# Kernel tuning notes

Hardware: AMD Instinct MI355X
Metric: run time of the kernel (lower is better)

The kernel has to match this reference:

```python
import jax, jax.numpy as jnp
import numpy as np

N_NODES = 100000
N_EDGES = 1600000
D_IN = 64
D_OUT = 64


def setup_inputs() -> dict:
    key = jax.random.key(0)
    k1, k2, k3, k4, k5 = jax.random.split(key, 5)
    x = jax.random.normal(k1, (N_NODES, D_IN), dtype=jnp.float32)
    edge_index = jax.random.randint(k2, (2, N_EDGES), 0, N_NODES, dtype=jnp.int64)
    dist_vec = jax.random.uniform(k3, (N_EDGES,), dtype=jnp.float32)
    # Linear params (xavier-uniform-like scale for W)
    limit = float(np.sqrt(6.0 / (D_IN + D_OUT)))
    W = jax.random.uniform(k4, (D_OUT, D_IN), minval=-limit, maxval=limit, dtype=jnp.float32)
    b = jax.random.uniform(k5, (D_OUT,), minval=-limit, maxval=limit, dtype=jnp.float32)
    return {"x": x, "edge_index": edge_index, "dist_vec": dist_vec, "W": W, "b": b}


def reference(x, edge_index, dist_vec, W, b):
    row, col = edge_index[0], edge_index[1]
    n = x.shape[0]
    # degree of destination (col) nodes
    deg = jax.ops.segment_sum(jnp.ones_like(dist_vec), col, num_segments=n)
    deg_inv_sqrt = jnp.where(deg > 0, jax.lax.rsqrt(deg), 0.0)
    norm = deg_inv_sqrt[row] * deg_inv_sqrt[col]  # [E]
    w = jnp.exp(-dist_vec ** 2) * norm            # [E]
    # sparse.mm(adj, x): out[row] += w * x[col]
    msgs = w[:, None] * x[col]                    # [E, D_IN]
    side_embed = jax.ops.segment_sum(msgs, row, num_segments=n)  # [N, D_IN]
    return side_embed @ W.T + b
```

## Files before the change

### kernel.cpp

```cpp
#include <hip/hip_runtime.h>
#include <hip/hip_fp16.h>


constexpr int NN   = 100000;
constexpr int NE   = 1600000;
constexpr int D    = 64;
constexpr int NRB  = (NN + 63) / 64;
constexpr int NCB  = (NN + 255) / 256;
constexpr int HB   = 250;
constexpr int HT   = 1024;
constexpr int CHUNK = NE / HB;
constexpr int NSR  = NRB * HB;
constexpr int NSCC = NCB * HB;
constexpr int NST  = NSR + NSCC;
constexpr int SCB  = 1024;
constexpr int SCG  = (NST + SCB - 1) / SCB;
constexpr int CAP  = 1536;

using f16x8 = __attribute__((ext_vector_type(8))) _Float16;
using f32x4 = __attribute__((ext_vector_type(4))) float;

__global__ void __launch_bounds__(HT)
hist2_kernel(const int* __restrict__ row, const int* __restrict__ col,
             int* __restrict__ hist) {
    __shared__ int hr[NRB], hc[NCB];
    const int t = threadIdx.x;
    for (int i = t; i < NRB; i += HT) hr[i] = 0;
    for (int i = t; i < NCB; i += HT) hc[i] = 0;
    __syncthreads();
    const int e0 = blockIdx.x * CHUNK;
    for (int e = e0 + t * 4; e < e0 + CHUNK; e += HT * 4) {
        const int4 r4 = *reinterpret_cast<const int4*>(row + e);
        const int4 c4 = *reinterpret_cast<const int4*>(col + e);
        atomicAdd(&hr[r4.x >> 6], 1); atomicAdd(&hr[r4.y >> 6], 1);
        atomicAdd(&hr[r4.z >> 6], 1); atomicAdd(&hr[r4.w >> 6], 1);
        atomicAdd(&hc[c4.x >> 8], 1); atomicAdd(&hc[c4.y >> 8], 1);
        atomicAdd(&hc[c4.z >> 8], 1); atomicAdd(&hc[c4.w >> 8], 1);
    }
    __syncthreads();
    for (int i = t; i < NRB; i += HT) hist[i * HB + blockIdx.x] = hr[i];
    for (int i = t; i < NCB; i += HT) hist[NSR + i * HB + blockIdx.x] = hc[i];
}

__global__ void scanpart_kernel(const int* __restrict__ a, int* __restrict__ bsum) {
    __shared__ int red[16];
    const int t = threadIdx.x;
    const int i = blockIdx.x * SCB + t;
    int s = (i < NST) ? a[i] : 0;
    #pragma unroll
    for (int o = 1; o < 64; o <<= 1) s += __shfl_xor(s, o);
    if ((t & 63) == 0) red[t >> 6] = s;
    __syncthreads();
    if (t < 16) {
        int ss = red[t];
        #pragma unroll
        for (int o = 1; o < 16; o <<= 1) ss += __shfl_xor(ss, o);
        if (t == 0) bsum[blockIdx.x] = ss;
    }
}

__global__ void scanfinal_kernel(int* __restrict__ a, const int* __restrict__ bsum) {
    __shared__ int wsum[16], wsum2[16], red[16];
    __shared__ int prefix_s;
    const int t = threadIdx.x;
    const int i = blockIdx.x * SCB + t;
    const int lane = t & 63;
    const int w = t >> 6;
    int pv = (t < blockIdx.x) ? bsum[t] : 0;
    #pragma unroll
    for (int o = 1; o < 64; o <<= 1) pv += __shfl_xor(pv, o);
    if (lane == 0) red[w] = pv;
    const int v = (i < NST) ? a[i] : 0;
    int s = v;
    #pragma unroll
    for (int o = 1; o < 64; o <<= 1) { int u = __shfl_up(s, o); if (lane >= o) s += u; }
    if (lane == 63) wsum[w] = s;
    __syncthreads();
    if (t < 16) {
        int ss = wsum[t];
        #pragma unroll
        for (int o = 1; o < 16; o <<= 1) { int u = __shfl_up(ss, o); if (t >= o) ss += u; }
        wsum2[t] = ss;
        int rr = red[t];
        #pragma unroll
        for (int o = 1; o < 16; o <<= 1) rr += __shfl_xor(rr, o);
        if (t == 0) prefix_s = rr;
    }
    __syncthreads();
    const int excl = prefix_s + (w ? wsum2[w - 1] : 0) + (s - v);
    if (i < NST) a[i] = excl;
}

__global__ void __launch_bounds__(HT)
scatboth_kernel(const int* __restrict__ row, const int* __restrict__ col,
                const float* __restrict__ dist, const int* __restrict__ hoff,
                unsigned* __restrict__ payload, unsigned char* __restrict__ colidx) {
    __shared__ int cur_r[NRB];
    __shared__ int cur_c[NCB];
    const int t = threadIdx.x;
    for (int i = t; i < NRB; i += HT) cur_r[i] = hoff[i * HB + blockIdx.x];
    for (int i = t; i < NCB; i += HT) cur_c[i] = hoff[NSR + i * HB + blockIdx.x] - NE;
    __syncthreads();
    const int e0 = blockIdx.x * CHUNK;
    for (int e = e0 + t * 4; e < e0 + CHUNK; e += HT * 4) {
        const int4 r4 = *reinterpret_cast<const int4*>(row + e);
        const int4 c4 = *reinterpret_cast<const int4*>(col + e);
        const float4 d4 = *reinterpret_cast<const float4*>(dist + e);
        const int rr[4] = {r4.x, r4.y, r4.z, r4.w};
        const int cc[4] = {c4.x, c4.y, c4.z, c4.w};
        const float dd[4] = {d4.x, d4.y, d4.z, d4.w};
        #pragma unroll
        for (int j = 0; j < 4; ++j) {
            const int r = rr[j];
            const int c = cc[j];
            const float dv = dd[j];
            const unsigned w8 = (unsigned)(__expf(-dv * dv) * 255.0f + 0.5f);
            const int pr = atomicAdd(&cur_r[r >> 6], 1);
            payload[pr] = ((unsigned)(r & 63) << 25) | (w8 << 17) | (unsigned)c;
            const int pc = atomicAdd(&cur_c[c >> 8], 1);
            colidx[pc] = (unsigned char)(c & 255);
        }
    }
}

__global__ void __launch_bounds__(256)
coldinv_kernel(const int* __restrict__ hoff, const unsigned char* __restrict__ colidx,
               float* __restrict__ dinv) {
    __shared__ int cnt[256];
    const int t = threadIdx.x;
    const int b = blockIdx.x;
    cnt[t] = 0;
    __syncthreads();
    const int s0 = hoff[NSR + b * HB] - NE;
    const int s1 = (b + 1 < NCB) ? (hoff[NSR + (b + 1) * HB] - NE) : NE;
    for (int k = s0 + t; k < s1; k += 256) atomicAdd(&cnt[colidx[k]], 1);
    __syncthreads();
    const int n = b * 256 + t;
    if (n < NN) {
        const int d = cnt[t];
        dinv[n] = (d > 0) ? rsqrtf((float)d) : 0.0f;
    }
}

__global__ void __launch_bounds__(256)
ygemm_kernel(const float* __restrict__ x, const float* __restrict__ W,
             __half* __restrict__ y) {
    const int t = threadIdx.x;
    const int m  = t & 15;
    const int kb = (t & 63) >> 4;
    f16x8 bf[4][2];
    #pragma unroll
    for (int jt = 0; jt < 4; ++jt) {
        #pragma unroll
        for (int kh = 0; kh < 2; ++kh) {
            const float* wp = W + (size_t)(jt * 16 + m) * 64 + kh * 32 + kb * 8;
            const float4 w0 = *reinterpret_cast<const float4*>(wp);
            const float4 w1 = *reinterpret_cast<const float4*>(wp + 4);
            f16x8 f;
            f[0] = (_Float16)w0.x; f[1] = (_Float16)w0.y;
            f[2] = (_Float16)w0.z; f[3] = (_Float16)w0.w;
            f[4] = (_Float16)w1.x; f[5] = (_Float16)w1.y;
            f[6] = (_Float16)w1.z; f[7] = (_Float16)w1.w;
            bf[jt][kh] = f;
        }
    }
    const int wid = (blockIdx.x * 256 + t) >> 6;
    const int nw  = (gridDim.x * 256) >> 6;
    for (int nt = wid; nt < NN / 16; nt += nw) {
        const int n0 = nt * 16;
        f16x8 af[2];
        #pragma unroll
        for (int kh = 0; kh < 2; ++kh) {
            const float* xp = x + (size_t)(n0 + m) * 64 + kh * 32 + kb * 8;
            const float4 x0 = *reinterpret_cast<const float4*>(xp);
            const float4 x1 = *reinterpret_cast<const float4*>(xp + 4);
            f16x8 f;
            f[0] = (_Float16)x0.x; f[1] = (_Float16)x0.y;
            f[2] = (_Float16)x0.z; f[3] = (_Float16)x0.w;
            f[4] = (_Float16)x1.x; f[5] = (_Float16)x1.y;
            f[6] = (_Float16)x1.z; f[7] = (_Float16)x1.w;
            af[kh] = f;
        }
        #pragma unroll
        for (int jt = 0; jt < 4; ++jt) {
            f32x4 acc = {0.f, 0.f, 0.f, 0.f};
            acc = __builtin_amdgcn_mfma_f32_16x16x32_f16(bf[jt][0], af[0], acc, 0, 0, 0);
            acc = __builtin_amdgcn_mfma_f32_16x16x32_f16(bf[jt][1], af[1], acc, 0, 0, 0);
            const size_t elem = (size_t)(n0 + m) * 64 + jt * 16 + kb * 4;
            union { uint2 u; __half h[4]; } pk;
            pk.h[0] = __float2half(acc[0]); pk.h[1] = __float2half(acc[1]);
            pk.h[2] = __float2half(acc[2]); pk.h[3] = __float2half(acc[3]);
            *reinterpret_cast<uint2*>(y + elem) = pk.u;
        }
    }
}

__global__ void __launch_bounds__(256)
gather_fused_kernel(const int* __restrict__ hoff, const unsigned* __restrict__ payload,
                    const float* __restrict__ dinvg, const __half* __restrict__ y,
                    const float* __restrict__ bias, float* __restrict__ out) {
    __shared__ unsigned stage[CAP];
    __shared__ unsigned sorted[CAP];
    __shared__ int cnt[64], cur[64], rs[65];
    __shared__ float dinv_s[64];
    const int t = threadIdx.x;
    const int lane = t & 63;
    const int wv = t >> 6;
    const int b = blockIdx.x;
    const int sub = lane >> 3;
    const int ch8 = (lane & 7) << 3;
    constexpr float WSCL = 1.0f / 255.0f;
    const float4 b0 = *reinterpret_cast<const float4*>(bias + ch8);
    const float4 b1 = *reinterpret_cast<const float4*>(bias + ch8 + 4);

    if (t < 64) {
        cnt[t] = 0;
        const int n = b * 64 + t;
        dinv_s[t] = (n < NN) ? dinvg[n] : 0.0f;
    }
    const int s0g = hoff[b * HB];
    const int s1g = (b + 1 < NRB) ? hoff[(b + 1) * HB] : NE;
    int ne = s1g - s0g;
    ne = (ne < CAP) ? ne : CAP;
    __syncthreads();
    for (int k = t; k < ne; k += 256) {
        const unsigned p = payload[s0g + k];
        stage[k] = p;
        atomicAdd(&cnt[p >> 25], 1);
    }
    __syncthreads();
    if (t < 64) {
        const int v = cnt[t];
        int s = v;
        #pragma unroll
        for (int o = 1; o < 64; o <<= 1) { int u = __shfl_up(s, o); if (t >= o) s += u; }
        cur[t] = s - v;
        rs[t] = s - v;
        if (t == 63) rs[64] = s;
    }
    __syncthreads();
    for (int k = t; k < ne; k += 256) {
        const unsigned p = stage[k];
        const int pos = atomicAdd(&cur[p >> 25], 1);
        sorted[pos] = p;
    }
    __syncthreads();

    for (int ln = wv; ln < 64; ln += 4) {
        const int n = b * 64 + ln;
        if (n >= NN) break;
        const int e0 = rs[ln];
        const int e1 = rs[ln + 1];
        float a0 = 0.f, a1 = 0.f, a2 = 0.f, a3 = 0.f;
        float a4 = 0.f, a5 = 0.f, a6 = 0.f, a7 = 0.f;
        for (int p0 = e0; p0 < e1; p0 += 8) {
            const int pp = p0 + sub;
            const int ppc = (pp < e1) ? pp : (e1 - 1);
            const unsigned m = sorted[ppc];
            const int c = (int)(m & 0x1FFFFu);
            float wgt = (float)((m >> 17) & 255u) * WSCL * dinvg[c];
            wgt = (pp < e1) ? wgt : 0.0f;
            const float4 raw = *reinterpret_cast<const float4*>(y + (size_t)c * 64 + ch8);
            const __half2* h2 = reinterpret_cast<const __half2*>(&raw);
            const float2 f0 = __half22float2(h2[0]);
            const float2 f1 = __half22float2(h2[1]);
            const float2 f2 = __half22float2(h2[2]);
            const float2 f3 = __half22float2(h2[3]);
            a0 += wgt * f0.x; a1 += wgt * f0.y; a2 += wgt * f1.x; a3 += wgt * f1.y;
            a4 += wgt * f2.x; a5 += wgt * f2.y; a6 += wgt * f3.x; a7 += wgt * f3.y;
        }
        #pragma unroll
        for (int o = 8; o < 64; o <<= 1) {
            a0 += __shfl_xor(a0, o); a1 += __shfl_xor(a1, o);
            a2 += __shfl_xor(a2, o); a3 += __shfl_xor(a3, o);
            a4 += __shfl_xor(a4, o); a5 += __shfl_xor(a5, o);
            a6 += __shfl_xor(a6, o); a7 += __shfl_xor(a7, o);
        }
        if (sub == 0) {
            const float dn = dinv_s[ln];
            const float4 o0 = make_float4(b0.x + dn * a0, b0.y + dn * a1,
                                          b0.z + dn * a2, b0.w + dn * a3);
            const float4 o1 = make_float4(b1.x + dn * a4, b1.y + dn * a5,
                                          b1.z + dn * a6, b1.w + dn * a7);
            float* op = out + (size_t)n * 64 + ch8;
            *reinterpret_cast<float4*>(op)     = o0;
            *reinterpret_cast<float4*>(op + 4) = o1;
        }
    }
}

extern "C" void kernel_launch(void* const* d_in, const int* in_sizes, int n_in,
                              void* d_out, int out_size, void* d_ws, size_t ws_size,
                              hipStream_t stream) {
    const float* x    = (const float*)d_in[0];
    const int*   ei   = (const int*)d_in[1];
    const float* dist = (const float*)d_in[2];
    const float* W    = (const float*)d_in[3];
    const float* b    = (const float*)d_in[4];
    float* out = (float*)d_out;

    const int* row = ei;
    const int* col = ei + NE;

    unsigned*      payload = (unsigned*)d_ws;
    __half*        y       = (__half*)(payload + NE);
    int*           hist    = (int*)(y + (size_t)NN * 64);
    int*           bsum    = hist + NST;
    unsigned char* colidx  = (unsigned char*)(bsum + SCG);
    float*         dinv    = (float*)(colidx + NE);

    ygemm_kernel    <<<1024, 256, 0, stream>>>(x, W, y);
    hist2_kernel    <<<HB, HT, 0, stream>>>(row, col, hist);
    scanpart_kernel <<<SCG, SCB, 0, stream>>>(hist, bsum);
    scanfinal_kernel<<<SCG, SCB, 0, stream>>>(hist, bsum);
    scatboth_kernel <<<HB, HT, 0, stream>>>(row, col, dist, hist, payload, colidx);
    coldinv_kernel  <<<NCB, 256, 0, stream>>>(hist, colidx, dinv);
    gather_fused_kernel<<<NRB, 256, 0, stream>>>(hist, payload, dinv, y, b, out);
}
```

Before: 117.5 us.

## Merge y-GEMM and edge histogram into one horizontally fused prep kernel

Combines the independent x·W^T fp16 MFMA kernel and the row/col block histogram kernel into a single launch. The first 250 blocks build the histograms and the next 512 blocks run the GEMM, so both independent jobs share the device at the same time and one launch is removed. Block size drops from 1024/256 to 512 for both roles. The histogram blocks now have fewer threads per chunk, and register pressure from the MFMA path may now apply to the histogram blocks as well.

```diff
diff --git a/kernel.cpp b/kernel.cpp
--- a/kernel.cpp
+++ b/kernel.cpp
@@ -9,6 +9,8 @@
 constexpr int NCB  = (NN + 255) / 256;
 constexpr int HB   = 250;
 constexpr int HT   = 1024;
+constexpr int PT   = 512;
+constexpr int YGB  = 512;
 constexpr int CHUNK = NE / HB;
 constexpr int NSR  = NRB * HB;
 constexpr int NSCC = NCB * HB;
@@ -20,26 +22,78 @@
 using f16x8 = __attribute__((ext_vector_type(8))) _Float16;
 using f32x4 = __attribute__((ext_vector_type(4))) float;
 
-__global__ void __launch_bounds__(HT)
-hist2_kernel(const int* __restrict__ row, const int* __restrict__ col,
-             int* __restrict__ hist) {
+__global__ void __launch_bounds__(PT)
+prep_kernel(const float* __restrict__ x, const float* __restrict__ W,
+            __half* __restrict__ y, const int* __restrict__ row,
+            const int* __restrict__ col, int* __restrict__ hist) {
     __shared__ int hr[NRB], hc[NCB];
     const int t = threadIdx.x;
-    for (int i = t; i < NRB; i += HT) hr[i] = 0;
-    for (int i = t; i < NCB; i += HT) hc[i] = 0;
-    __syncthreads();
-    const int e0 = blockIdx.x * CHUNK;
-    for (int e = e0 + t * 4; e < e0 + CHUNK; e += HT * 4) {
-        const int4 r4 = *reinterpret_cast<const int4*>(row + e);
-        const int4 c4 = *reinterpret_cast<const int4*>(col + e);
-        atomicAdd(&hr[r4.x >> 6], 1); atomicAdd(&hr[r4.y >> 6], 1);
-        atomicAdd(&hr[r4.z >> 6], 1); atomicAdd(&hr[r4.w >> 6], 1);
-        atomicAdd(&hc[c4.x >> 8], 1); atomicAdd(&hc[c4.y >> 8], 1);
-        atomicAdd(&hc[c4.z >> 8], 1); atomicAdd(&hc[c4.w >> 8], 1);
-    }
-    __syncthreads();
-    for (int i = t; i < NRB; i += HT) hist[i * HB + blockIdx.x] = hr[i];
-    for (int i = t; i < NCB; i += HT) hist[NSR + i * HB + blockIdx.x] = hc[i];
+    const int blk = blockIdx.x;
+    if (blk < HB) {
+        for (int i = t; i < NRB; i += PT) hr[i] = 0;
+        for (int i = t; i < NCB; i += PT) hc[i] = 0;
+        __syncthreads();
+        const int e0 = blk * CHUNK;
+        for (int e = e0 + t * 4; e < e0 + CHUNK; e += PT * 4) {
+            const int4 r4 = *reinterpret_cast<const int4*>(row + e);
+            const int4 c4 = *reinterpret_cast<const int4*>(col + e);
+            atomicAdd(&hr[r4.x >> 6], 1); atomicAdd(&hr[r4.y >> 6], 1);
+            atomicAdd(&hr[r4.z >> 6], 1); atomicAdd(&hr[r4.w >> 6], 1);
+            atomicAdd(&hc[c4.x >> 8], 1); atomicAdd(&hc[c4.y >> 8], 1);
+            atomicAdd(&hc[c4.z >> 8], 1); atomicAdd(&hc[c4.w >> 8], 1);
+        }
+        __syncthreads();
+        for (int i = t; i < NRB; i += PT) hist[i * HB + blk] = hr[i];
+        for (int i = t; i < NCB; i += PT) hist[NSR + i * HB + blk] = hc[i];
+    } else {
+        const int m  = t & 15;
+        const int kb = (t & 63) >> 4;
+        f16x8 bf[4][2];
+        #pragma unroll
+        for (int jt = 0; jt < 4; ++jt) {
+            #pragma unroll
+            for (int kh = 0; kh < 2; ++kh) {
+                const float* wp = W + (size_t)(jt * 16 + m) * 64 + kh * 32 + kb * 8;
+                const float4 w0 = *reinterpret_cast<const float4*>(wp);
+                const float4 w1 = *reinterpret_cast<const float4*>(wp + 4);
+                f16x8 f;
+                f[0] = (_Float16)w0.x; f[1] = (_Float16)w0.y;
+                f[2] = (_Float16)w0.z; f[3] = (_Float16)w0.w;
+                f[4] = (_Float16)w1.x; f[5] = (_Float16)w1.y;
+                f[6] = (_Float16)w1.z; f[7] = (_Float16)w1.w;
+                bf[jt][kh] = f;
+            }
+        }
+        const int wid = ((blk - HB) * PT + t) >> 6;
+        const int nw  = (YGB * PT) >> 6;
+        for (int nt = wid; nt < NN / 16; nt += nw) {
+            const int n0 = nt * 16;
+            f16x8 af[2];
+            #pragma unroll
+            for (int kh = 0; kh < 2; ++kh) {
+                const float* xp = x + (size_t)(n0 + m) * 64 + kh * 32 + kb * 8;
+                const float4 x0 = *reinterpret_cast<const float4*>(xp);
+                const float4 x1 = *reinterpret_cast<const float4*>(xp + 4);
+                f16x8 f;
+                f[0] = (_Float16)x0.x; f[1] = (_Float16)x0.y;
+                f[2] = (_Float16)x0.z; f[3] = (_Float16)x0.w;
+                f[4] = (_Float16)x1.x; f[5] = (_Float16)x1.y;
+                f[6] = (_Float16)x1.z; f[7] = (_Float16)x1.w;
+                af[kh] = f;
+            }
+            #pragma unroll
+            for (int jt = 0; jt < 4; ++jt) {
+                f32x4 acc = {0.f, 0.f, 0.f, 0.f};
+                acc = __builtin_amdgcn_mfma_f32_16x16x32_f16(bf[jt][0], af[0], acc, 0, 0, 0);
+                acc = __builtin_amdgcn_mfma_f32_16x16x32_f16(bf[jt][1], af[1], acc, 0, 0, 0);
+                const size_t elem = (size_t)(n0 + m) * 64 + jt * 16 + kb * 4;
+                union { uint2 u; __half h[4]; } pk;
+                pk.h[0] = __float2half(acc[0]); pk.h[1] = __float2half(acc[1]);
+                pk.h[2] = __float2half(acc[2]); pk.h[3] = __float2half(acc[3]);
+                *reinterpret_cast<uint2*>(y + elem) = pk.u;
+            }
+        }
+    }
 }
 
 __global__ void scanpart_kernel(const int* __restrict__ a, int* __restrict__ bsum) {
@@ -139,59 +193,6 @@
     if (n < NN) {
         const int d = cnt[t];
         dinv[n] = (d > 0) ? rsqrtf((float)d) : 0.0f;
-    }
-}
-
-__global__ void __launch_bounds__(256)
-ygemm_kernel(const float* __restrict__ x, const float* __restrict__ W,
-             __half* __restrict__ y) {
-    const int t = threadIdx.x;
-    const int m  = t & 15;
-    const int kb = (t & 63) >> 4;
-    f16x8 bf[4][2];
-    #pragma unroll
-    for (int jt = 0; jt < 4; ++jt) {
-        #pragma unroll
-        for (int kh = 0; kh < 2; ++kh) {
-            const float* wp = W + (size_t)(jt * 16 + m) * 64 + kh * 32 + kb * 8;
-            const float4 w0 = *reinterpret_cast<const float4*>(wp);
-            const float4 w1 = *reinterpret_cast<const float4*>(wp + 4);
-            f16x8 f;
-            f[0] = (_Float16)w0.x; f[1] = (_Float16)w0.y;
-            f[2] = (_Float16)w0.z; f[3] = (_Float16)w0.w;
-            f[4] = (_Float16)w1.x; f[5] = (_Float16)w1.y;
-            f[6] = (_Float16)w1.z; f[7] = (_Float16)w1.w;
-            bf[jt][kh] = f;
-        }
-    }
-    const int wid = (blockIdx.x * 256 + t) >> 6;
-    const int nw  = (gridDim.x * 256) >> 6;
-    for (int nt = wid; nt < NN / 16; nt += nw) {
-        const int n0 = nt * 16;
-        f16x8 af[2];
-        #pragma unroll
-        for (int kh = 0; kh < 2; ++kh) {
-            const float* xp = x + (size_t)(n0 + m) * 64 + kh * 32 + kb * 8;
-            const float4 x0 = *reinterpret_cast<const float4*>(xp);
-            const float4 x1 = *reinterpret_cast<const float4*>(xp + 4);
-            f16x8 f;
-            f[0] = (_Float16)x0.x; f[1] = (_Float16)x0.y;
-            f[2] = (_Float16)x0.z; f[3] = (_Float16)x0.w;
-            f[4] = (_Float16)x1.x; f[5] = (_Float16)x1.y;
-            f[6] = (_Float16)x1.z; f[7] = (_Float16)x1.w;
-            af[kh] = f;
-        }
-        #pragma unroll
-        for (int jt = 0; jt < 4; ++jt) {
-            f32x4 acc = {0.f, 0.f, 0.f, 0.f};
-            acc = __builtin_amdgcn_mfma_f32_16x16x32_f16(bf[jt][0], af[0], acc, 0, 0, 0);
-            acc = __builtin_amdgcn_mfma_f32_16x16x32_f16(bf[jt][1], af[1], acc, 0, 0, 0);
-            const size_t elem = (size_t)(n0 + m) * 64 + jt * 16 + kb * 4;
-            union { uint2 u; __half h[4]; } pk;
-            pk.h[0] = __float2half(acc[0]); pk.h[1] = __float2half(acc[1]);
-            pk.h[2] = __float2half(acc[2]); pk.h[3] = __float2half(acc[3]);
-            *reinterpret_cast<uint2*>(y + elem) = pk.u;
-        }
     }
 }
 
@@ -309,8 +310,7 @@
     unsigned char* colidx  = (unsigned char*)(bsum + SCG);
     float*         dinv    = (float*)(colidx + NE);
 
-    ygemm_kernel    <<<1024, 256, 0, stream>>>(x, W, y);
-    hist2_kernel    <<<HB, HT, 0, stream>>>(row, col, hist);
+    prep_kernel     <<<HB + YGB, PT, 0, stream>>>(x, W, y, row, col, hist);
     scanpart_kernel <<<SCG, SCB, 0, stream>>>(hist, bsum);
     scanfinal_kernel<<<SCG, SCB, 0, stream>>>(hist, bsum);
     scatboth_kernel <<<HB, HT, 0, stream>>>(row, col, dist, hist, payload, colidx);
```

Result: faster. 114.3 us (-2.7%).
